# Performance work log

Hardware: AMD Instinct MI355X
Metric: run time of the kernel (lower is better)

The kernel has to match this reference:

```python
import jax, jax.numpy as jnp
import numpy as np

D_MODEL = 1024
N_HEADS = 16
HEAD_DIM = D_MODEL // N_HEADS


def setup_inputs() -> dict:
    key = jax.random.key(0)
    ks = jax.random.split(key, 5)
    B, S = 4, 2048
    scale = 1.0 / np.sqrt(D_MODEL)
    return {
        "x": jax.random.normal(ks[0], (B, S, D_MODEL), dtype=jnp.float32),
        "W_q": jax.random.normal(ks[1], (D_MODEL, D_MODEL), dtype=jnp.float32) * scale,
        "W_k": jax.random.normal(ks[2], (D_MODEL, D_MODEL), dtype=jnp.float32) * scale,
        "W_v": jax.random.normal(ks[3], (D_MODEL, D_MODEL), dtype=jnp.float32) * scale,
        "W_o": jax.random.normal(ks[4], (D_MODEL, D_MODEL), dtype=jnp.float32) * scale,
    }


def reference(x, W_q, W_k, W_v, W_o):
    B, S, _ = x.shape
    # nn.Linear(d,d,bias=False): y = x @ W.T ; W stored as (out,in)
    def proj(W):
        y = jnp.einsum('bsd,ed->bse', x, W)
        return y.reshape(B, S, N_HEADS, HEAD_DIM).transpose(0, 2, 1, 3)  # (B,H,S,Dh)
    q, k, v = proj(W_q), proj(W_k), proj(W_v)
    scores = jnp.einsum('bhqd,bhkd->bhqk', q, k) / np.sqrt(HEAD_DIM)
    causal = jnp.tril(jnp.ones((S, S), dtype=bool))  # (S,S)
    scores = jnp.where(causal[None, None], scores, -jnp.inf)
    attn = jax.nn.softmax(scores, axis=-1)
    heads = jnp.einsum('bhqk,bhkd->bhqd', attn, v)
    concat = heads.transpose(0, 2, 1, 3).reshape(B, S, D_MODEL)
    return jnp.einsum('bsd,ed->bse', concat, W_o)
```

## Files before the change

### kernel.cpp

```cpp
#include <hip/hip_runtime.h>
#include <hip/hip_bf16.h>

#define D_MODEL 1024
#define N_HEADS 16
#define HEAD_DIM 64
#define BATCH 4
#define SEQ 2048
#define M_ROWS (BATCH * SEQ)

typedef __attribute__((ext_vector_type(8))) __bf16 bf16x8;
typedef __attribute__((ext_vector_type(8))) short short8;
typedef __attribute__((ext_vector_type(4))) float f32x4;

static __device__ __forceinline__ unsigned short f2bf_rne(float f) {
  unsigned int u = __float_as_uint(f);
  u += 0x7FFFu + ((u >> 16) & 1u);
  return (unsigned short)(u >> 16);
}

static __device__ __forceinline__ unsigned int cvtpk_bf16(float a, float b) {
  unsigned int r;
  asm("v_cvt_pk_bf16_f32 %0, %1, %2" : "=v"(r) : "v"(a), "v"(b));
  return r;
}

#if __has_builtin(__builtin_amdgcn_exp2f)
#define EXP2F(x) __builtin_amdgcn_exp2f(x)
#else
#define EXP2F(x) exp2f(x)
#endif

static __device__ __forceinline__ void gl_lds16(const unsigned short* g, unsigned short* l) {
  __builtin_amdgcn_global_load_lds((const __attribute__((address_space(1))) unsigned int*)g,
                                   (__attribute__((address_space(3))) unsigned int*)l, 16, 0, 0);
}

#define BAR() asm volatile("s_barrier" ::: "memory")
#define WAIT_LGKM0() asm volatile("s_waitcnt lgkmcnt(0)" ::: "memory")
#define WAIT_VM(N) asm volatile("s_waitcnt vmcnt(" #N ")" ::: "memory")

__global__ __launch_bounds__(256) void cvt_all(const float* __restrict__ x,
                                               const float* __restrict__ wq,
                                               const float* __restrict__ wk,
                                               const float* __restrict__ wv,
                                               const float* __restrict__ wo,
                                               unsigned short* __restrict__ xb,
                                               unsigned short* __restrict__ wqb,
                                               unsigned short* __restrict__ wkb,
                                               unsigned short* __restrict__ wvb,
                                               unsigned short* __restrict__ wob) {
  const int bid = blockIdx.x;
  const float* src;
  unsigned short* dst;
  int i;
  if (bid < 8192) {
    src = x; dst = xb; i = bid * 256 + threadIdx.x;
  } else {
    int r = bid - 8192;
    int w = r >> 10;
    i = (r & 1023) * 256 + threadIdx.x;
    switch (w) {
      case 0: src = wq; dst = wqb; break;
      case 1: src = wk; dst = wkb; break;
      case 2: src = wv; dst = wvb; break;
      default: src = wo; dst = wob; break;
    }
  }
  float4 f = reinterpret_cast<const float4*>(src)[i];
  ushort4 o;
  o.x = f2bf_rne(f.x); o.y = f2bf_rne(f.y); o.z = f2bf_rne(f.z); o.w = f2bf_rne(f.w);
  reinterpret_cast<ushort4*>(dst)[i] = o;
}

__global__ __launch_bounds__(512, 2) void qk_gemm8(const unsigned short* __restrict__ A,
                                                   const unsigned short* __restrict__ Wq,
                                                   const unsigned short* __restrict__ Wk,
                                                   unsigned short* __restrict__ Qo,
                                                   unsigned short* __restrict__ Ko) {
  __shared__ __align__(16) unsigned short smem[65536];

  const int bid = blockIdx.x;
  const int wgid = (bid & 7) * 32 + (bid >> 3);
  const int widx = wgid >> 7;
  const int rem = wgid & 127;
  const int bm = rem >> 2, bn = rem & 3;

  const unsigned short* Bw = (widx == 0) ? Wq : Wk;

  const int t = threadIdx.x;
  const int wave = t >> 6, lane = t & 63;
  const int wmi = wave >> 2, wni = wave & 3;
  const int lr = lane & 15, quad = lane >> 4;

  const int r0 = t >> 3, c0 = (t & 7) ^ (r0 & 7);
  const int s1 = t + 512;
  const int r1 = s1 >> 3, c1 = (s1 & 7) ^ (r1 & 7);
  const unsigned short* Asrc0 = A + (size_t)(bm * 256 + r0) * D_MODEL + c0 * 8;
  const unsigned short* Asrc1 = A + (size_t)(bm * 256 + r1) * D_MODEL + c1 * 8;
  const unsigned short* Bsrc0 = Bw + (size_t)(bn * 256 + r0) * D_MODEL + c0 * 8;
  const unsigned short* Bsrc1 = Bw + (size_t)(bn * 256 + r1) * D_MODEL + c1 * 8;

  auto stageA = [&](int kt, int buf, int half) {
    unsigned short* dst = &smem[(buf * 2 + half) * 8192];
    const size_t go = (size_t)half * (128 * D_MODEL) + kt * 64;
    gl_lds16(Asrc0 + go, dst + t * 8);
    gl_lds16(Asrc1 + go, dst + s1 * 8);
  };
  auto stageB = [&](int kt, int buf, int half) {
    unsigned short* dst = &smem[32768 + (buf * 2 + half) * 8192];
    const size_t go = (size_t)half * (128 * D_MODEL) + kt * 64;
    gl_lds16(Bsrc0 + go, dst + t * 8);
    gl_lds16(Bsrc1 + go, dst + s1 * 8);
  };

  f32x4 acc[8][4] = {};
  bf16x8 bfrag[4][2];

  stageA(0, 0, 0); stageA(0, 0, 1);
  stageB(0, 0, 0); stageB(0, 0, 1);
  stageB(1, 1, 0); stageB(1, 1, 1);
  WAIT_VM(4);
  BAR();

  const int brow0 = (wni & 1) * 64;
  for (int j = 0; j < 8; ++j) {
#pragma unroll
    for (int tb = 0; tb < 2; ++tb) {
      const unsigned short* As = &smem[(tb * 2 + wmi) * 8192];
      const unsigned short* Bs = &smem[32768 + (tb * 2 + (wni >> 1)) * 8192];
#pragma unroll
      for (int qd = 0; qd < 4; ++qd) {
        const int p = tb * 4 + qd;
        if (qd == 0) {
#pragma unroll
          for (int n = 0; n < 4; ++n)
#pragma unroll
            for (int ks = 0; ks < 2; ++ks) {
              const int row = brow0 + n * 16 + lr;
              bfrag[n][ks] = __builtin_bit_cast(
                  bf16x8, *reinterpret_cast<const short8*>(
                              &Bs[row * 64 + (((ks * 4 + quad) ^ (row & 7)) * 8)]));
            }
        }
        bf16x8 af[2][2];
#pragma unroll
        for (int mi = 0; mi < 2; ++mi)
#pragma unroll
          for (int ks = 0; ks < 2; ++ks) {
            const int row = (qd * 2 + mi) * 16 + lr;
            af[mi][ks] = __builtin_bit_cast(
                bf16x8, *reinterpret_cast<const short8*>(
                            &As[row * 64 + (((ks * 4 + quad) ^ (row & 7)) * 8)]));
          }
        if (p == 0) stageA(2 * j + 1, 1, 0);
        if (p == 1) { stageA(2 * j + 1, 1, 1); if (j < 7) stageB(2 * j + 2, 0, 0); }
        if (p == 2) { if (j < 7) stageB(2 * j + 2, 0, 1); }
        if (p == 4) { if (j < 7) stageA(2 * j + 2, 0, 0); }
        if (p == 5) { if (j < 7) { stageA(2 * j + 2, 0, 1); stageB(2 * j + 3, 1, 0); } }
        if (p == 6) { if (j < 7) stageB(2 * j + 3, 1, 1); }
        BAR();
        WAIT_LGKM0();
        __builtin_amdgcn_s_setprio(1);
#pragma unroll
        for (int mi = 0; mi < 2; ++mi)
#pragma unroll
          for (int n = 0; n < 4; ++n)
#pragma unroll
            for (int ks = 0; ks < 2; ++ks)
              acc[qd * 2 + mi][n] = __builtin_amdgcn_mfma_f32_16x16x32_bf16(
                  af[mi][ks], bfrag[n][ks], acc[qd * 2 + mi][n], 0, 0, 0);
        __builtin_amdgcn_s_setprio(0);
        if (p == 3) { if (j < 7) { WAIT_VM(4); } else { WAIT_VM(0); } }
        if (p == 7) { if (j < 7) { WAIT_VM(4); } }
        BAR();
      }
    }
  }

  unsigned short* Cp = (widx == 0) ? Qo : Ko;
  const float sc = (widx == 0) ? 0.18033688f : 1.0f;
#pragma unroll
  for (int m = 0; m < 8; ++m) {
#pragma unroll
    for (int n = 0; n < 4; ++n) {
      const int col = bn * 256 + wni * 64 + n * 16 + lr;
#pragma unroll
      for (int r = 0; r < 4; ++r) {
        const int row = bm * 256 + wmi * 128 + m * 16 + quad * 4 + r;
        Cp[(size_t)row * D_MODEL + col] = f2bf_rne(acc[m][n][r] * sc);
      }
    }
  }
}

__global__ __launch_bounds__(256) void v_gemm(const unsigned short* __restrict__ A,
                                              const unsigned short* __restrict__ Bw,
                                              unsigned short* __restrict__ Vt) {
  __shared__ __align__(16) unsigned short smem[16384];
  const int t = threadIdx.x;
  const int bn = blockIdx.x, bm = blockIdx.y;
  const int K = D_MODEL;
  const int wave = t >> 6, lane = t & 63;
  const int wm = (wave >> 1) * 64, wn = (wave & 1) * 64;
  const int lr = lane & 15, quad = lane >> 4;
  const int rxor = (lr >> 1) & 3;

  const int g0 = wave * 128 + lane, g1 = g0 + 64;
  const int r0 = g0 >> 2, c0 = (((g0 & 3) ^ ((r0 >> 1) & 3)) << 3);
  const int r1 = g1 >> 2, c1 = (((g1 & 3) ^ ((r1 >> 1) & 3)) << 3);
  const unsigned short* Arow0 = A + (size_t)(bm * 128 + r0) * K + c0;
  const unsigned short* Arow1 = A + (size_t)(bm * 128 + r1) * K + c1;
  const unsigned short* Brow0 = Bw + (size_t)(bn * 128 + r0) * K + c0;
  const unsigned short* Brow1 = Bw + (size_t)(bn * 128 + r1) * K + c1;

  f32x4 acc[4][4] = {};

  gl_lds16(Arow0, &smem[g0 * 8]);
  gl_lds16(Arow1, &smem[g1 * 8]);
  gl_lds16(Brow0, &smem[4096 + g0 * 8]);
  gl_lds16(Brow1, &smem[4096 + g1 * 8]);
  __syncthreads();

  for (int it = 0; it < 32; it++) {
    const int cur = (it & 1) * 8192;
    if (it + 1 < 32) {
      const int nxt = 8192 - cur;
      const int k1 = (it + 1) * 32;
      gl_lds16(Arow0 + k1, &smem[nxt + g0 * 8]);
      gl_lds16(Arow1 + k1, &smem[nxt + g1 * 8]);
      gl_lds16(Brow0 + k1, &smem[nxt + 4096 + g0 * 8]);
      gl_lds16(Brow1 + k1, &smem[nxt + 4096 + g1 * 8]);
    }
    const unsigned short* As = &smem[cur];
    const unsigned short* Bs = &smem[cur + 4096];

    bf16x8 af[4], bfr[4];
#pragma unroll
    for (int mt = 0; mt < 4; mt++)
      af[mt] = __builtin_bit_cast(
          bf16x8,
          *reinterpret_cast<const short8*>(&As[(wm + mt * 16 + lr) * 32 + (quad ^ rxor) * 8]));
#pragma unroll
    for (int nt = 0; nt < 4; nt++)
      bfr[nt] = __builtin_bit_cast(
          bf16x8,
          *reinterpret_cast<const short8*>(&Bs[(wn + nt * 16 + lr) * 32 + (quad ^ rxor) * 8]));
#pragma unroll
    for (int mt = 0; mt < 4; mt++)
#pragma unroll
      for (int nt = 0; nt < 4; nt++)
        acc[mt][nt] = __builtin_amdgcn_mfma_f32_16x16x32_bf16(af[mt], bfr[nt], acc[mt][nt], 0, 0, 0);
    __syncthreads();
  }

  const int b = bm >> 4;
  const int s0 = (bm & 15) * 128;
#pragma unroll
  for (int half = 0; half < 2; half++) {
    __syncthreads();
    if ((wave & 1) == half) {
#pragma unroll
      for (int nt = 0; nt < 4; nt++) {
#pragma unroll
        for (int mt = 0; mt < 4; mt++) {
#pragma unroll
          for (int r = 0; r < 4; r++) {
            int cl = nt * 16 + lr;
            int rl = wm + mt * 16 + quad * 4 + r;
            smem[cl * 136 + rl] = f2bf_rne(acc[mt][nt][r]);
          }
        }
      }
    }
    __syncthreads();
    const int h2 = bn * 2 + half;
    const size_t rowbase = ((size_t)(b * N_HEADS + h2)) * HEAD_DIM;
#pragma unroll
    for (int i = 0; i < 4; i++) {
      int c = i * 256 + t;
      int d = c >> 4, s8 = (c & 15) * 8;
      uint4 v = *reinterpret_cast<const uint4*>(&smem[d * 136 + s8]);
      *reinterpret_cast<uint4*>(Vt + (rowbase + d) * SEQ + s0 + s8) = v;
    }
  }
}

__global__ __launch_bounds__(256) void gemm_bt_f32(const unsigned short* __restrict__ A,
                                                   const unsigned short* __restrict__ Bw,
                                                   float* __restrict__ Cp,
                                                   int M, int N, int K) {
  __shared__ __align__(16) unsigned short smem[16384];
  const int t = threadIdx.x;
  const int bn = blockIdx.x, bm = blockIdx.y;
  const int wave = t >> 6, lane = t & 63;
  const int wm = (wave >> 1) * 64, wn = (wave & 1) * 64;
  const int lr = lane & 15, quad = lane >> 4;
  const int rxor = (lr >> 1) & 3;

  const int g0 = wave * 128 + lane, g1 = g0 + 64;
  const int r0 = g0 >> 2, c0 = (((g0 & 3) ^ ((r0 >> 1) & 3)) << 3);
  const int r1 = g1 >> 2, c1 = (((g1 & 3) ^ ((r1 >> 1) & 3)) << 3);
  const unsigned short* Arow0 = A + (size_t)(bm * 128 + r0) * K + c0;
  const unsigned short* Arow1 = A + (size_t)(bm * 128 + r1) * K + c1;
  const unsigned short* Brow0 = Bw + (size_t)(bn * 128 + r0) * K + c0;
  const unsigned short* Brow1 = Bw + (size_t)(bn * 128 + r1) * K + c1;

  f32x4 acc[4][4] = {};

  gl_lds16(Arow0, &smem[g0 * 8]);
  gl_lds16(Arow1, &smem[g1 * 8]);
  gl_lds16(Brow0, &smem[4096 + g0 * 8]);
  gl_lds16(Brow1, &smem[4096 + g1 * 8]);
  __syncthreads();

  for (int it = 0; it < 32; it++) {
    const int cur = (it & 1) * 8192;
    if (it + 1 < 32) {
      const int nxt = 8192 - cur;
      const int k1 = (it + 1) * 32;
      gl_lds16(Arow0 + k1, &smem[nxt + g0 * 8]);
      gl_lds16(Arow1 + k1, &smem[nxt + g1 * 8]);
      gl_lds16(Brow0 + k1, &smem[nxt + 4096 + g0 * 8]);
      gl_lds16(Brow1 + k1, &smem[nxt + 4096 + g1 * 8]);
    }
    const unsigned short* As = &smem[cur];
    const unsigned short* Bs = &smem[cur + 4096];

    bf16x8 af[4], bfr[4];
#pragma unroll
    for (int mt = 0; mt < 4; mt++)
      af[mt] = __builtin_bit_cast(
          bf16x8,
          *reinterpret_cast<const short8*>(&As[(wm + mt * 16 + lr) * 32 + (quad ^ rxor) * 8]));
#pragma unroll
    for (int nt = 0; nt < 4; nt++)
      bfr[nt] = __builtin_bit_cast(
          bf16x8,
          *reinterpret_cast<const short8*>(&Bs[(wn + nt * 16 + lr) * 32 + (quad ^ rxor) * 8]));
#pragma unroll
    for (int mt = 0; mt < 4; mt++)
#pragma unroll
      for (int nt = 0; nt < 4; nt++)
        acc[mt][nt] = __builtin_amdgcn_mfma_f32_16x16x32_bf16(af[mt], bfr[nt], acc[mt][nt], 0, 0, 0);
    __syncthreads();
  }

#pragma unroll
  for (int mt = 0; mt < 4; mt++) {
#pragma unroll
    for (int nt = 0; nt < 4; nt++) {
      int col = bn * 128 + wn + nt * 16 + lr;
#pragma unroll
      for (int r = 0; r < 4; r++) {
        int row = bm * 128 + wm + mt * 16 + quad * 4 + r;
        Cp[(size_t)row * N + col] = acc[mt][nt][r];
      }
    }
  }
}

__global__ __launch_bounds__(512, 4) void attn_causal(const unsigned short* __restrict__ Q,
                                                      const unsigned short* __restrict__ Km,
                                                      const unsigned short* __restrict__ Vt,
                                                      unsigned short* __restrict__ O) {
  __shared__ __align__(16) unsigned short Kv[2][2][64 * 64];
  __shared__ __align__(16) unsigned short Ps[8][1024];

  const int bid = blockIdx.x;
  const int xcd = bid & 7, g = bid >> 3;
  const int p = g >> 3;
  const int bh = xcd * 8 + (g & 7);
  const int h = bh & 15;
  const int b = bh >> 4;

  const int t = threadIdx.x;
  const int wave = t >> 6, lane = t & 63;
  const int lr = lane & 15, quad = lane >> 4;
  const int cxor = lr & 7;

  const size_t base = (size_t)b * SEQ * D_MODEL + h * HEAD_DIM;
  const unsigned short* Qb = Q + base;
  const unsigned short* Kb = Km + base;
  const unsigned short* Vb = Vt + (size_t)(b * N_HEADS + h) * HEAD_DIM * SEQ;
  unsigned short* pw = &Ps[wave][0];

  const int srow = t >> 3;
  const int scol = ((t & 7) ^ (srow & 7)) << 3;
  const unsigned short* Kg = Kb + (size_t)srow * D_MODEL + scol;
  const unsigned short* Vg = Vb + (size_t)srow * SEQ + scol;

  for (int ph = 0; ph < 2; ph++) {
    const int qt = ph ? (15 - p) : p;
    const int m0 = qt * 128 + wave * 16;
    const int ntiles = (qt + 1) * 2;

    bf16x8 qf[2];
#pragma unroll
    for (int kk = 0; kk < 2; kk++)
      qf[kk] = __builtin_bit_cast(
          bf16x8,
          *reinterpret_cast<const short8*>(Qb + (size_t)(m0 + lr) * D_MODEL + kk * 32 + quad * 8));

    f32x4 o_acc[4] = {};
    float lsum = 0.f;

    gl_lds16(Kg, &Kv[0][0][t * 8]);
    gl_lds16(Vg, &Kv[0][1][t * 8]);

    for (int kt = 0; kt < ntiles; kt++) {
      const int cur = kt & 1;
      const int kv0 = kt * 64;
      __syncthreads();
      if (kt + 1 < ntiles) {
        gl_lds16(Kg + (size_t)(kv0 + 64) * D_MODEL, &Kv[1 - cur][0][t * 8]);
        gl_lds16(Vg + kv0 + 64, &Kv[1 - cur][1][t * 8]);
      }
      const unsigned short* Ks = &Kv[cur][0][0];
      const unsigned short* Vs = &Kv[cur][1][0];

      f32x4 sAcc[4] = {};
      __builtin_amdgcn_s_setprio(1);
#pragma unroll
      for (int kk = 0; kk < 2; kk++) {
        bf16x8 kf[4];
#pragma unroll
        for (int j = 0; j < 4; j++)
          kf[j] = __builtin_bit_cast(
              bf16x8, *reinterpret_cast<const short8*>(
                          &Ks[(j * 16 + lr) * 64 + ((kk * 4 + quad) ^ cxor) * 8]));
#pragma unroll
        for (int j = 0; j < 4; j++)
          sAcc[j] = __builtin_amdgcn_mfma_f32_16x16x32_bf16(kf[j], qf[kk], sAcc[j], 0, 0, 0);
      }
      __builtin_amdgcn_s_setprio(0);

      WAIT_LGKM0();
      const bool needmask = (kv0 + 63 > m0);
      const int kbase = kv0 - m0 + quad * 4;
#pragma unroll
      for (int j = 0; j < 4; j++) {
        float e[4];
#pragma unroll
        for (int r = 0; r < 4; r++) e[r] = EXP2F(sAcc[j][r]);
        if (needmask) {
#pragma unroll
          for (int r = 0; r < 4; r++)
            if (kbase + 16 * j + r > lr) e[r] = 0.f;
        }
        lsum += (e[0] + e[1]) + (e[2] + e[3]);
        const unsigned int pk0 = cvtpk_bf16(e[0], e[1]);
        const unsigned int pk1 = cvtpk_bf16(e[2], e[3]);
        const int c = 4 * j + quad;
        *reinterpret_cast<uint2*>(
            &pw[lr * 64 + (((c >> 1) ^ (lr & 7)) << 3) + ((c & 1) << 2)]) =
            make_uint2(pk0, pk1);
      }
      WAIT_LGKM0();

      __builtin_amdgcn_s_setprio(1);
#pragma unroll
      for (int kk = 0; kk < 2; kk++) {
        bf16x8 pf = __builtin_bit_cast(
            bf16x8, *reinterpret_cast<const short8*>(
                        &pw[lr * 64 + (((kk * 4 + quad) ^ (lr & 7)) << 3)]));
#pragma unroll
        for (int c = 0; c < 4; c++) {
          bf16x8 vv = __builtin_bit_cast(
              bf16x8, *reinterpret_cast<const short8*>(
                          &Vs[(c * 16 + lr) * 64 + ((kk * 4 + quad) ^ cxor) * 8]));
          o_acc[c] = __builtin_amdgcn_mfma_f32_16x16x32_bf16(pf, vv, o_acc[c], 0, 0, 0);
        }
      }
      __builtin_amdgcn_s_setprio(0);
    }

    float l = lsum;
    l += __shfl_xor(l, 16, 64);
    l += __shfl_xor(l, 32, 64);
#pragma unroll
    for (int r = 0; r < 4; r++) {
      const float lq = __shfl(l, quad * 4 + r, 16);
      const float inv = 1.f / lq;
      const int qpos = m0 + quad * 4 + r;
#pragma unroll
      for (int c = 0; c < 4; c++)
        O[base + (size_t)qpos * D_MODEL + c * 16 + lr] = f2bf_rne(o_acc[c][r] * inv);
    }
  }
}

extern "C" void kernel_launch(void* const* d_in, const int* in_sizes, int n_in,
                              void* d_out, int out_size, void* d_ws, size_t ws_size,
                              hipStream_t stream) {
  const float* x  = (const float*)d_in[0];
  const float* Wq = (const float*)d_in[1];
  const float* Wk = (const float*)d_in[2];
  const float* Wv = (const float*)d_in[3];
  const float* Wo = (const float*)d_in[4];
  float* out = (float*)d_out;

  char* ws = (char*)d_ws;
  const size_t SZ_X = (size_t)M_ROWS * D_MODEL * 2;
  const size_t SZ_W = (size_t)D_MODEL * D_MODEL * 2;
  unsigned short* xb  = (unsigned short*)(ws);
  unsigned short* wqb = (unsigned short*)(ws + SZ_X);
  unsigned short* wkb = (unsigned short*)(ws + SZ_X + 1 * SZ_W);
  unsigned short* wvb = (unsigned short*)(ws + SZ_X + 2 * SZ_W);
  unsigned short* wob = (unsigned short*)(ws + SZ_X + 3 * SZ_W);
  unsigned short* Qb  = (unsigned short*)(ws + 1 * SZ_X + 4 * SZ_W);
  unsigned short* Kb  = (unsigned short*)(ws + 2 * SZ_X + 4 * SZ_W);
  unsigned short* Vt  = (unsigned short*)(ws + 3 * SZ_X + 4 * SZ_W);
  unsigned short* Ob  = xb;

  cvt_all<<<12288, 256, 0, stream>>>(x, Wq, Wk, Wv, Wo, xb, wqb, wkb, wvb, wob);

  qk_gemm8<<<256, 512, 0, stream>>>(xb, wqb, wkb, Qb, Kb);

  v_gemm<<<dim3(8, 64), 256, 0, stream>>>(xb, wvb, Vt);

  attn_causal<<<512, 512, 0, stream>>>(Qb, Kb, Vt, Ob);

  gemm_bt_f32<<<dim3(8, 64), 256, 0, stream>>>(Ob, wob, out, M_ROWS, D_MODEL, D_MODEL);
}
```

Baseline: 232.9 us.

## Process two query sub-tiles per wave in causal attention to reuse K/V tiles

```diff
diff --git a/kernel.cpp b/kernel.cpp
--- a/kernel.cpp
+++ b/kernel.cpp
@@ -359,12 +359,12 @@
   }
 }
 
-__global__ __launch_bounds__(512, 4) void attn_causal(const unsigned short* __restrict__ Q,
+__global__ __launch_bounds__(512, 2) void attn_causal(const unsigned short* __restrict__ Q,
                                                       const unsigned short* __restrict__ Km,
                                                       const unsigned short* __restrict__ Vt,
                                                       unsigned short* __restrict__ O) {
   __shared__ __align__(16) unsigned short Kv[2][2][64 * 64];
-  __shared__ __align__(16) unsigned short Ps[8][1024];
+  __shared__ __align__(16) unsigned short Ps[8][2048];
 
   const int bid = blockIdx.x;
   const int xcd = bid & 7, g = bid >> 3;
@@ -382,7 +382,8 @@
   const unsigned short* Qb = Q + base;
   const unsigned short* Kb = Km + base;
   const unsigned short* Vb = Vt + (size_t)(b * N_HEADS + h) * HEAD_DIM * SEQ;
-  unsigned short* pw = &Ps[wave][0];
+  unsigned short* pwA = &Ps[wave][0];
+  unsigned short* pwB = &Ps[wave][1024];
 
   const int srow = t >> 3;
   const int scol = ((t & 7) ^ (srow & 7)) << 3;
@@ -390,35 +391,43 @@
   const unsigned short* Vg = Vb + (size_t)srow * SEQ + scol;
 
   for (int ph = 0; ph < 2; ph++) {
-    const int qt = ph ? (15 - p) : p;
-    const int m0 = qt * 128 + wave * 16;
-    const int ntiles = (qt + 1) * 2;
-
-    bf16x8 qf[2];
-#pragma unroll
-    for (int kk = 0; kk < 2; kk++)
-      qf[kk] = __builtin_bit_cast(
+    const int q256 = ph ? (7 - p) : p;
+    const int m0A = q256 * 256 + wave * 16;
+    const int m0B = m0A + 128;
+    const int nt = (q256 + 1) * 4;
+
+    bf16x8 qfA[2], qfB[2];
+#pragma unroll
+    for (int kk = 0; kk < 2; kk++) {
+      qfA[kk] = __builtin_bit_cast(
           bf16x8,
-          *reinterpret_cast<const short8*>(Qb + (size_t)(m0 + lr) * D_MODEL + kk * 32 + quad * 8));
-
-    f32x4 o_acc[4] = {};
-    float lsum = 0.f;
+          *reinterpret_cast<const short8*>(Qb + (size_t)(m0A + lr) * D_MODEL + kk * 32 + quad * 8));
+      qfB[kk] = __builtin_bit_cast(
+          bf16x8,
+          *reinterpret_cast<const short8*>(Qb + (size_t)(m0B + lr) * D_MODEL + kk * 32 + quad * 8));
+    }
+
+    f32x4 oA[4] = {}, oB[4] = {};
+    float lsA = 0.f, lsB = 0.f;
 
     gl_lds16(Kg, &Kv[0][0][t * 8]);
     gl_lds16(Vg, &Kv[0][1][t * 8]);
 
-    for (int kt = 0; kt < ntiles; kt++) {
+    for (int kt = 0; kt < nt; kt++) {
       const int cur = kt & 1;
       const int kv0 = kt * 64;
       __syncthreads();
-      if (kt + 1 < ntiles) {
+      if (kt + 1 < nt) {
         gl_lds16(Kg + (size_t)(kv0 + 64) * D_MODEL, &Kv[1 - cur][0][t * 8]);
         gl_lds16(Vg + kv0 + 64, &Kv[1 - cur][1][t * 8]);
       }
       const unsigned short* Ks = &Kv[cur][0][0];
       const unsigned short* Vs = &Kv[cur][1][0];
 
-      f32x4 sAcc[4] = {};
+      const bool doA = (kv0 <= m0A + 15);
+      const bool doB = (kv0 <= m0B + 15);
+
+      f32x4 sA[4] = {}, sB[4] = {};
       __builtin_amdgcn_s_setprio(1);
 #pragma unroll
       for (int kk = 0; kk < 2; kk++) {
@@ -428,64 +437,88 @@
           kf[j] = __builtin_bit_cast(
               bf16x8, *reinterpret_cast<const short8*>(
                           &Ks[(j * 16 + lr) * 64 + ((kk * 4 + quad) ^ cxor) * 8]));
-#pragma unroll
-        for (int j = 0; j < 4; j++)
-          sAcc[j] = __builtin_amdgcn_mfma_f32_16x16x32_bf16(kf[j], qf[kk], sAcc[j], 0, 0, 0);
+        if (doA) {
+#pragma unroll
+          for (int j = 0; j < 4; j++)
+            sA[j] = __builtin_amdgcn_mfma_f32_16x16x32_bf16(kf[j], qfA[kk], sA[j], 0, 0, 0);
+        }
+        if (doB) {
+#pragma unroll
+          for (int j = 0; j < 4; j++)
+            sB[j] = __builtin_amdgcn_mfma_f32_16x16x32_bf16(kf[j], qfB[kk], sB[j], 0, 0, 0);
+        }
       }
       __builtin_amdgcn_s_setprio(0);
 
       WAIT_LGKM0();
-      const bool needmask = (kv0 + 63 > m0);
-      const int kbase = kv0 - m0 + quad * 4;
-#pragma unroll
-      for (int j = 0; j < 4; j++) {
-        float e[4];
-#pragma unroll
-        for (int r = 0; r < 4; r++) e[r] = EXP2F(sAcc[j][r]);
-        if (needmask) {
-#pragma unroll
-          for (int r = 0; r < 4; r++)
-            if (kbase + 16 * j + r > lr) e[r] = 0.f;
+
+      auto softmax_store = [&](const f32x4* s, int m0, unsigned short* pw, float& lsum) {
+        const bool needmask = (kv0 + 63 > m0);
+        const int kbase = kv0 - m0 + quad * 4;
+#pragma unroll
+        for (int j = 0; j < 4; j++) {
+          float e[4];
+#pragma unroll
+          for (int r = 0; r < 4; r++) e[r] = EXP2F(s[j][r]);
+          if (needmask) {
+#pragma unroll
+            for (int r = 0; r < 4; r++)
+              if (kbase + 16 * j + r > lr) e[r] = 0.f;
+          }
+          lsum += (e[0] + e[1]) + (e[2] + e[3]);
+          const unsigned int pk0 = cvtpk_bf16(e[0], e[1]);
+          const unsigned int pk1 = cvtpk_bf16(e[2], e[3]);
+          const int c = 4 * j + quad;
+          *reinterpret_cast<uint2*>(
+              &pw[lr * 64 + (((c >> 1) ^ (lr & 7)) << 3) + ((c & 1) << 2)]) =
+              make_uint2(pk0, pk1);
         }
-        lsum += (e[0] + e[1]) + (e[2] + e[3]);
-        const unsigned int pk0 = cvtpk_bf16(e[0], e[1]);
-        const unsigned int pk1 = cvtpk_bf16(e[2], e[3]);
-        const int c = 4 * j + quad;
-        *reinterpret_cast<uint2*>(
-            &pw[lr * 64 + (((c >> 1) ^ (lr & 7)) << 3) + ((c & 1) << 2)]) =
-            make_uint2(pk0, pk1);
-      }
+      };
+      if (doA) softmax_store(sA, m0A, pwA, lsA);
+      if (doB) softmax_store(sB, m0B, pwB, lsB);
+
       WAIT_LGKM0();
 
       __builtin_amdgcn_s_setprio(1);
 #pragma unroll
       for (int kk = 0; kk < 2; kk++) {
-        bf16x8 pf = __builtin_bit_cast(
-            bf16x8, *reinterpret_cast<const short8*>(
-                        &pw[lr * 64 + (((kk * 4 + quad) ^ (lr & 7)) << 3)]));
+        bf16x8 pfA = {}, pfB = {};
+        if (doA)
+          pfA = __builtin_bit_cast(
+              bf16x8, *reinterpret_cast<const short8*>(
+                          &pwA[lr * 64 + (((kk * 4 + quad) ^ (lr & 7)) << 3)]));
+        if (doB)
+          pfB = __builtin_bit_cast(
+              bf16x8, *reinterpret_cast<const short8*>(
+                          &pwB[lr * 64 + (((kk * 4 + quad) ^ (lr & 7)) << 3)]));
 #pragma unroll
         for (int c = 0; c < 4; c++) {
           bf16x8 vv = __builtin_bit_cast(
               bf16x8, *reinterpret_cast<const short8*>(
                           &Vs[(c * 16 + lr) * 64 + ((kk * 4 + quad) ^ cxor) * 8]));
-          o_acc[c] = __builtin_amdgcn_mfma_f32_16x16x32_bf16(pf, vv, o_acc[c], 0, 0, 0);
+          if (doA) oA[c] = __builtin_amdgcn_mfma_f32_16x16x32_bf16(pfA, vv, oA[c], 0, 0, 0);
+          if (doB) oB[c] = __builtin_amdgcn_mfma_f32_16x16x32_bf16(pfB, vv, oB[c], 0, 0, 0);
         }
       }
       __builtin_amdgcn_s_setprio(0);
     }
 
-    float l = lsum;
-    l += __shfl_xor(l, 16, 64);
-    l += __shfl_xor(l, 32, 64);
-#pragma unroll
-    for (int r = 0; r < 4; r++) {
-      const float lq = __shfl(l, quad * 4 + r, 16);
-      const float inv = 1.f / lq;
-      const int qpos = m0 + quad * 4 + r;
-#pragma unroll
-      for (int c = 0; c < 4; c++)
-        O[base + (size_t)qpos * D_MODEL + c * 16 + lr] = f2bf_rne(o_acc[c][r] * inv);
-    }
+    auto finish = [&](float lsum, const f32x4* o, int m0) {
+      float l = lsum;
+      l += __shfl_xor(l, 16, 64);
+      l += __shfl_xor(l, 32, 64);
+#pragma unroll
+      for (int r = 0; r < 4; r++) {
+        const float lq = __shfl(l, quad * 4 + r, 16);
+        const float inv = 1.f / lq;
+        const int qpos = m0 + quad * 4 + r;
+#pragma unroll
+        for (int c = 0; c < 4; c++)
+          O[base + (size_t)qpos * D_MODEL + c * 16 + lr] = f2bf_rne(o[c][r] * inv);
+      }
+    };
+    finish(lsA, oA, m0A);
+    finish(lsB, oB, m0B);
   }
 }
 
@@ -518,7 +551,7 @@
 
   v_gemm<<<dim3(8, 64), 256, 0, stream>>>(xb, wvb, Vt);
 
-  attn_causal<<<512, 512, 0, stream>>>(Qb, Kb, Vt, Ob);
+  attn_causal<<<256, 512, 0, stream>>>(Qb, Kb, Vt, Ob);
 
   gemm_bt_f32<<<dim3(8, 64), 256, 0, stream>>>(Ob, wob, out, M_ROWS, D_MODEL, D_MODEL);
 }
```

After: 253.9 us. +9.0%, slower.
